# Performance work log

Hardware: AMD Instinct MI355X
Metric: run time of the kernel (lower is better)

## Reference

```python
import jax, jax.numpy as jnp
import numpy as np

C = 256
NUM_HEADS = 4
GROUPS = 32  # max(1, 256//8), divides 256
EPS = 1e-5


def setup_inputs() -> dict:
    key = jax.random.key(0)
    ks = jax.random.split(key, 7)
    B, H, W = 4, 64, 64
    s = 0.02
    return {
        "x": jax.random.normal(ks[0], (B, C, H, W), dtype=jnp.float32),
        "norm_gamma": jnp.ones((C,), jnp.float32),
        "norm_beta": jnp.zeros((C,), jnp.float32),
        "qkv_w": jax.random.normal(ks[1], (3 * C, C), jnp.float32) * s,  # 1x1 conv kernel squeezed
        "qkv_b": jax.random.normal(ks[2], (3 * C,), jnp.float32) * s,
        "proj_w": jax.random.normal(ks[3], (C, C), jnp.float32) * s,
        "proj_b": jax.random.normal(ks[4], (C,), jnp.float32) * s,
    }


def reference(x, norm_gamma, norm_beta, qkv_w, qkv_b, proj_w, proj_b):
    B, Cc, H, W = x.shape
    hd = Cc // NUM_HEADS
    scale = hd ** -0.5

    # GroupNorm over (channels-per-group, H, W)
    xg = x.reshape(B, GROUPS, Cc // GROUPS, H, W)
    mu = xg.mean(axis=(2, 3, 4), keepdims=True)
    var = xg.var(axis=(2, 3, 4), keepdims=True)
    h = ((xg - mu) * jax.lax.rsqrt(var + EPS)).reshape(B, Cc, H, W)
    h = h * norm_gamma[:, None, None] + norm_beta[:, None, None]

    # 1x1 conv QKV: [B,3C,H,W]
    qkv = jnp.einsum('bchw,oc->bohw', h, qkv_w) + qkv_b[:, None, None]
    q, k, v = jnp.split(qkv, 3, axis=1)

    def heads(t):  # [B,C,H,W] -> [B,nh,HW,hd]
        return t.reshape(B, NUM_HEADS, hd, H * W).transpose(0, 1, 3, 2)

    q, k, v = heads(q), heads(k), heads(v)
    attn = jnp.einsum('bhnd,bhmd->bhnm', q, k) * scale  # [B,nh,HW,HW]
    attn = jax.nn.softmax(attn, axis=-1)
    out = jnp.einsum('bhnm,bhmd->bhnd', attn, v)  # [B,nh,HW,hd]
    out = out.transpose(0, 1, 3, 2).reshape(B, Cc, H, W)

    out = jnp.einsum('bchw,oc->bohw', out, proj_w) + proj_b[:, None, None]
    return x + out
```

## Files before the change

kernel.cpp:

```cpp
#include <hip/hip_runtime.h>
#include <hip/hip_bf16.h>
#include <stdint.h>

typedef unsigned short u16;
typedef __attribute__((ext_vector_type(8))) short bf16x8;
typedef __attribute__((ext_vector_type(4))) float f32x4;
typedef __attribute__((ext_vector_type(16))) float f32x16;

#define HW 4096
#define CC 256
#define QSCALE 0.18033688011112042f

__device__ __forceinline__ u16 f2bf(float f) {
    union { float f; uint32_t i; } v; v.f = f;
    uint32_t x = v.i;
    return (u16)((x + 0x7fffu + ((x >> 16) & 1u)) >> 16);
}

__device__ __forceinline__ float fast_exp2(float x) {
#if __has_builtin(__builtin_amdgcn_exp2f)
    return __builtin_amdgcn_exp2f(x);
#else
    return exp2f(x);
#endif
}

__device__ __forceinline__ unsigned cvt_pk_bf16(float lo, float hi) {
    unsigned r;
    asm("v_cvt_pk_bf16_f32 %0, %1, %2" : "=v"(r) : "v"(lo), "v"(hi));
    return r;
}

__device__ __forceinline__ void plane_swap(unsigned& a, unsigned& b) {
#if __has_builtin(__builtin_amdgcn_permlane32_swap)
    auto r = __builtin_amdgcn_permlane32_swap(a, b, false, false);
    a = r[0]; b = r[1];
#else
    unsigned ax = __shfl_xor((int)a, 32);
    unsigned bx = __shfl_xor((int)b, 32);
    bool hi = (threadIdx.x & 32) != 0;
    unsigned na = hi ? bx : a;
    unsigned nb = hi ? b : ax;
    a = na; b = nb;
#endif
}

#define MFMA16(a, b, c) __builtin_amdgcn_mfma_f32_16x16x32_bf16(a, b, c, 0, 0, 0)
#define MFMA32(a, b, c) __builtin_amdgcn_mfma_f32_32x32x16_bf16(a, b, c, 0, 0, 0)

__global__ void k_wsc(const float* __restrict__ qkv_w, const float* __restrict__ proj_w,
                      const float* __restrict__ x,
                      u16* __restrict__ wqkv, u16* __restrict__ wproj, float* __restrict__ stats) {
    int bid = blockIdx.x;
    if (bid < 128) {
        int bg = bid;
        const float4* p = reinterpret_cast<const float4*>(x + (size_t)bg * 8 * HW);
        float s = 0.f, ss = 0.f;
        for (int i = 0; i < 32; ++i) {
            float4 v = p[threadIdx.x + i * 256];
            s += v.x + v.y + v.z + v.w;
            ss += v.x * v.x + v.y * v.y + v.z * v.z + v.w * v.w;
        }
        __shared__ float rs[256], rss[256];
        rs[threadIdx.x] = s; rss[threadIdx.x] = ss;
        __syncthreads();
        for (int off = 128; off > 0; off >>= 1) {
            if (threadIdx.x < off) { rs[threadIdx.x] += rs[threadIdx.x + off]; rss[threadIdx.x] += rss[threadIdx.x + off]; }
            __syncthreads();
        }
        if (threadIdx.x == 0) {
            float mu = rs[0] * (1.f / 32768.f);
            float var = rss[0] * (1.f / 32768.f) - mu * mu;
            stats[bg * 2] = mu;
            stats[bg * 2 + 1] = rsqrtf(var + 1e-5f);
        }
    } else {
        int i = (bid - 128) * 256 + threadIdx.x;
        if (i < 768 * 256) {
            int o = i >> 8;
            float sc = (o < 256) ? QSCALE : 1.0f;
            wqkv[i] = f2bf(qkv_w[i] * sc);
        }
        int j = i - 768 * 256;
        if (j >= 0 && j < 256 * 256) wproj[j] = f2bf(proj_w[j]);
    }
}

__global__ __launch_bounds__(256) void k_gnt(const float* __restrict__ x, const float* __restrict__ stats,
                                             const float* __restrict__ gamma, const float* __restrict__ beta,
                                             u16* __restrict__ h_t) {
    int bid = blockIdx.x;
    int b = bid >> 8;
    int cb = (bid >> 6) & 3;
    int nb = bid & 63;
    int t = threadIdx.x;
    int cl = t >> 2;
    int ch = t & 3;
    int c = cb * 64 + cl;
    int g = c >> 3;
    float mu = stats[(b * 32 + g) * 2];
    float rsg = stats[(b * 32 + g) * 2 + 1];
    float ga = gamma[c], be = beta[c];
    __shared__ float T[64][66];
    const float4* p = reinterpret_cast<const float4*>(x + ((size_t)(b * CC + c)) * HW + nb * 64 + ch * 16);
    for (int j = 0; j < 4; ++j) {
        float4 v = p[j];
        int nbase = ch * 16 + j * 4;
        T[nbase + 0][cl] = (v.x - mu) * rsg * ga + be;
        T[nbase + 1][cl] = (v.y - mu) * rsg * ga + be;
        T[nbase + 2][cl] = (v.z - mu) * rsg * ga + be;
        T[nbase + 3][cl] = (v.w - mu) * rsg * ga + be;
    }
    __syncthreads();
    int nl = t >> 2;
    union { u16 u[16]; uint4 q[2]; } pk;
    for (int j = 0; j < 16; ++j) pk.u[j] = f2bf(T[nl][ch * 16 + j]);
    u16* dst = h_t + ((size_t)b * HW + nb * 64 + nl) * CC + cb * 64 + ch * 16;
    *reinterpret_cast<uint4*>(dst) = pk.q[0];
    *reinterpret_cast<uint4*>(dst + 8) = pk.q[1];
}

__global__ __launch_bounds__(256) void k_qkv(const u16* __restrict__ wqkv, const u16* __restrict__ h_t,
                                             const float* __restrict__ qkv_b,
                                             u16* __restrict__ qk_t, u16* __restrict__ v_o) {
    int bid = blockIdx.x;
    int b = bid / 192;
    int rem = bid % 192;
    int om = rem >> 5;
    int nb = rem & 31;
    int o0 = om * 128, n0 = nb * 128;
    int t = threadIdx.x;
    int wid = t >> 6, lane = t & 63;
    int wm = wid >> 1, wn = wid & 1;
    int l15 = lane & 15, lg = lane >> 4;

    __shared__ u16 sA[128 * 40], sB[128 * 40];
    f32x4 acc[4][4];
    for (int i = 0; i < 4; ++i) for (int j = 0; j < 4; ++j) acc[i][j] = (f32x4)0.f;

    const u16* gA = wqkv + (size_t)o0 * 256;
    const u16* gB = h_t + ((size_t)b * HW + n0) * CC;
    int row = t >> 1, half = t & 1;

    for (int kt = 0; kt < 8; ++kt) {
        __syncthreads();
        {
            const uint4* pa = reinterpret_cast<const uint4*>(gA + (size_t)row * 256 + kt * 32 + half * 16);
            uint4 a0 = pa[0], a1 = pa[1];
            const uint4* pb = reinterpret_cast<const uint4*>(gB + (size_t)row * 256 + kt * 32 + half * 16);
            uint4 b0 = pb[0], b1 = pb[1];
            *reinterpret_cast<uint4*>(&sA[row * 40 + half * 16]) = a0;
            *reinterpret_cast<uint4*>(&sA[row * 40 + half * 16 + 8]) = a1;
            *reinterpret_cast<uint4*>(&sB[row * 40 + half * 16]) = b0;
            *reinterpret_cast<uint4*>(&sB[row * 40 + half * 16 + 8]) = b1;
        }
        __syncthreads();
        bf16x8 af[4], bfr[4];
        for (int mt = 0; mt < 4; ++mt)
            af[mt] = *reinterpret_cast<const bf16x8*>(&sA[(wm * 64 + mt * 16 + l15) * 40 + lg * 8]);
        for (int nt = 0; nt < 4; ++nt)
            bfr[nt] = *reinterpret_cast<const bf16x8*>(&sB[(wn * 64 + nt * 16 + l15) * 40 + lg * 8]);
        for (int mt = 0; mt < 4; ++mt)
            for (int nt = 0; nt < 4; ++nt)
                acc[mt][nt] = MFMA16(af[mt], bfr[nt], acc[mt][nt]);
    }

    if (o0 < 512) {
        for (int mt = 0; mt < 4; ++mt) {
            int ob = o0 + wm * 64 + mt * 16 + lg * 4;
            float bias[4];
            for (int r = 0; r < 4; ++r) {
                int o = ob + r;
                bias[r] = qkv_b[o] * (o < 256 ? QSCALE : 1.0f);
            }
            for (int nt = 0; nt < 4; ++nt) {
                int n = n0 + wn * 64 + nt * 16 + l15;
                union { u16 u[4]; uint2 q; } pk;
                for (int r = 0; r < 4; ++r) pk.u[r] = f2bf(acc[mt][nt][r] + bias[r]);
                *reinterpret_cast<uint2*>(qk_t + ((size_t)b * HW + n) * 512 + ob) = pk.q;
            }
        }
    } else {
        for (int mt = 0; mt < 4; ++mt) {
            int ob = o0 + wm * 64 + mt * 16 + lg * 4;
            for (int nt = 0; nt < 4; ++nt) {
                int n = n0 + wn * 64 + nt * 16 + l15;
                for (int r = 0; r < 4; ++r) {
                    int o = ob + r;
                    float bias = qkv_b[o];
                    v_o[((size_t)b * 256 + (o - 512)) * HW + n] = f2bf(acc[mt][nt][r] + bias);
                }
            }
        }
    }
}

__global__ __launch_bounds__(512, 4) void k_attn(const u16* __restrict__ qk_t, const u16* __restrict__ v_o,
                                                 u16* __restrict__ ao_t) {
    int bid = blockIdx.x;
    int swz = (bid & 7) * 64 + (bid >> 3);
    int qb = swz & 31, head = (swz >> 5) & 3, b = swz >> 7;
    int n0 = qb * 128;
    int t = threadIdx.x;
    int kg = t >> 8;
    int wq = (t >> 6) & 3;
    int lane = t & 63, l31 = lane & 31, h = lane >> 5;

    __shared__ u16 lds[2 * 2 * 2 * 64 * 72];

    const u16* qbase = qk_t + ((size_t)b * HW + n0 + wq * 32 + l31) * 512 + head * 64 + h * 8;
    bf16x8 qf[4];
#pragma unroll
    for (int cs = 0; cs < 4; ++cs) qf[cs] = *reinterpret_cast<const bf16x8*>(qbase + cs * 16);

    const u16* gK = qk_t + (size_t)b * HW * 512 + 256 + head * 64;
    const u16* gV = v_o + ((size_t)b * 256 + head * 64) * (size_t)HW;

    int tIn = t & 255;
    int srow = tIn >> 3, sch = tIn & 7;
    const u16* pk0 = gK + (size_t)(kg * 2048 + srow) * 512 + sch * 8;
    const u16* pk1 = pk0 + 32 * 512;
    const u16* pv0 = gV + (size_t)srow * HW + kg * 2048 + sch * 8;
    const u16* pv1 = pv0 + 32 * HW;
    uint4 rk0 = *reinterpret_cast<const uint4*>(pk0);
    uint4 rk1 = *reinterpret_cast<const uint4*>(pk1);
    uint4 rv0 = *reinterpret_cast<const uint4*>(pv0);
    uint4 rv1 = *reinterpret_cast<const uint4*>(pv1);

    f32x16 o0 = (f32x16)0.f, o1 = (f32x16)0.f;
    float l_run = 0.f;
    u16* gb = lds + kg * 18432;

    for (int ti = 0; ti < 32; ++ti) {
        u16* bK = gb + (ti & 1) * 9216;
        u16* bV = bK + 4608;
        *reinterpret_cast<uint4*>(bK + srow * 72 + sch * 8) = rk0;
        *reinterpret_cast<uint4*>(bK + (srow + 32) * 72 + sch * 8) = rk1;
        *reinterpret_cast<uint4*>(bV + srow * 72 + sch * 8) = rv0;
        *reinterpret_cast<uint4*>(bV + (srow + 32) * 72 + sch * 8) = rv1;
        __syncthreads();

        if (ti < 31) {
            pk0 += 64 * 512; pk1 += 64 * 512; pv0 += 64; pv1 += 64;
            rk0 = *reinterpret_cast<const uint4*>(pk0);
            rk1 = *reinterpret_cast<const uint4*>(pk1);
            rv0 = *reinterpret_cast<const uint4*>(pv0);
            rv1 = *reinterpret_cast<const uint4*>(pv1);
        }

        f32x16 s0 = (f32x16)0.f, s1 = (f32x16)0.f;
        __builtin_amdgcn_s_setprio(1);
#pragma unroll
        for (int cs = 0; cs < 4; ++cs) {
            bf16x8 k0 = *reinterpret_cast<const bf16x8*>(bK + l31 * 72 + cs * 16 + h * 8);
            bf16x8 k1 = *reinterpret_cast<const bf16x8*>(bK + (l31 + 32) * 72 + cs * 16 + h * 8);
            s0 = MFMA32(k0, qf[cs], s0);
            s1 = MFMA32(k1, qf[cs], s1);
        }
        __builtin_amdgcn_s_setprio(0);

        float ps = 0.f;
#pragma unroll
        for (int i = 0; i < 16; ++i) { float e = fast_exp2(s0[i]); s0[i] = e; ps += e; }
#pragma unroll
        for (int i = 0; i < 16; ++i) { float e = fast_exp2(s1[i]); s1[i] = e; ps += e; }
        l_run += ps;

        unsigned dws[2][8];
#pragma unroll
        for (int a = 0; a < 4; ++a) {
            dws[0][2 * a]     = cvt_pk_bf16(s0[4 * a],     s0[4 * a + 1]);
            dws[0][2 * a + 1] = cvt_pk_bf16(s0[4 * a + 2], s0[4 * a + 3]);
            dws[1][2 * a]     = cvt_pk_bf16(s1[4 * a],     s1[4 * a + 1]);
            dws[1][2 * a + 1] = cvt_pk_bf16(s1[4 * a + 2], s1[4 * a + 3]);
        }
        bf16x8 pf[4];
#pragma unroll
        for (int ks = 0; ks < 4; ++ks) {
            int kt = ks >> 1, sf = ks & 1;
            unsigned A0 = dws[kt][4 * sf + 0], B0 = dws[kt][4 * sf + 2];
            unsigned A1 = dws[kt][4 * sf + 1], B1 = dws[kt][4 * sf + 3];
            plane_swap(A0, B0);
            plane_swap(A1, B1);
            union { unsigned d[4]; bf16x8 v; } u;
            u.d[0] = A0; u.d[1] = A1; u.d[2] = B0; u.d[3] = B1;
            pf[ks] = u.v;
        }

        __builtin_amdgcn_s_setprio(1);
#pragma unroll
        for (int ks = 0; ks < 4; ++ks) {
            bf16x8 v0 = *reinterpret_cast<const bf16x8*>(bV + l31 * 72 + ks * 16 + h * 8);
            bf16x8 v1 = *reinterpret_cast<const bf16x8*>(bV + (l31 + 32) * 72 + ks * 16 + h * 8);
            o0 = MFMA32(v0, pf[ks], o0);
            o1 = MFMA32(v1, pf[ks], o1);
        }
        __builtin_amdgcn_s_setprio(0);
    }

    l_run += __shfl_xor(l_run, 32);

    float* Of = (float*)lds;
    float* Lf = (float*)lds + 8192;
    u16* E = lds + 18432;

    __syncthreads();
    if (kg == 1) {
#pragma unroll
        for (int i = 0; i < 16; ++i) {
            Of[wq * 2048 + i * 64 + lane] = o0[i];
            Of[wq * 2048 + (16 + i) * 64 + lane] = o1[i];
        }
        Lf[wq * 64 + lane] = l_run;
    }
    __syncthreads();
    if (kg == 0) {
#pragma unroll
        for (int i = 0; i < 16; ++i) {
            o0[i] += Of[wq * 2048 + i * 64 + lane];
            o1[i] += Of[wq * 2048 + (16 + i) * 64 + lane];
        }
        l_run += Lf[wq * 64 + lane];
        float inv = 1.0f / l_run;
        int qrow = wq * 32 + l31;
#pragma unroll
        for (int r = 0; r < 16; ++r) {
            int d = (r & 3) + 8 * (r >> 2) + 4 * h;
            E[qrow * 72 + d]      = f2bf(o0[r] * inv);
            E[qrow * 72 + 32 + d] = f2bf(o1[r] * inv);
        }
    }
    __syncthreads();
#pragma unroll
    for (int i = 0; i < 2; ++i) {
        int item = i * 512 + t;
        int row = item >> 3, cb = item & 7;
        uint4 w = *reinterpret_cast<const uint4*>(E + row * 72 + cb * 8);
        *reinterpret_cast<uint4*>(ao_t + ((size_t)b * HW + n0 + row) * 256 + head * 64 + cb * 8) = w;
    }
}

__global__ __launch_bounds__(256) void k_proj(const u16* __restrict__ wproj, const u16* __restrict__ ao_t,
                                              const float* __restrict__ proj_b, const float* __restrict__ x,
                                              float* __restrict__ out) {
    int bid = blockIdx.x;
    int b = bid >> 6;
    int om = (bid >> 5) & 1;
    int nb = bid & 31;
    int o0 = om * 128, n0 = nb * 128;
    int t = threadIdx.x;
    int wid = t >> 6, lane = t & 63;
    int wm = wid >> 1, wn = wid & 1;
    int l15 = lane & 15, lg = lane >> 4;

    __shared__ u16 sA[128 * 40], sB[128 * 40];
    f32x4 acc[4][4];
    for (int i = 0; i < 4; ++i) for (int j = 0; j < 4; ++j) acc[i][j] = (f32x4)0.f;

    const u16* gA = wproj + (size_t)o0 * 256;
    const u16* gB = ao_t + ((size_t)b * HW + n0) * CC;
    int row = t >> 1, half = t & 1;

    for (int kt = 0; kt < 8; ++kt) {
        __syncthreads();
        {
            const uint4* pa = reinterpret_cast<const uint4*>(gA + (size_t)row * 256 + kt * 32 + half * 16);
            uint4 a0 = pa[0], a1 = pa[1];
            const uint4* pb = reinterpret_cast<const uint4*>(gB + (size_t)row * 256 + kt * 32 + half * 16);
            uint4 b0 = pb[0], b1 = pb[1];
            *reinterpret_cast<uint4*>(&sA[row * 40 + half * 16]) = a0;
            *reinterpret_cast<uint4*>(&sA[row * 40 + half * 16 + 8]) = a1;
            *reinterpret_cast<uint4*>(&sB[row * 40 + half * 16]) = b0;
            *reinterpret_cast<uint4*>(&sB[row * 40 + half * 16 + 8]) = b1;
        }
        __syncthreads();
        bf16x8 af[4], bfr[4];
        for (int mt = 0; mt < 4; ++mt)
            af[mt] = *reinterpret_cast<const bf16x8*>(&sA[(wm * 64 + mt * 16 + l15) * 40 + lg * 8]);
        for (int nt = 0; nt < 4; ++nt)
            bfr[nt] = *reinterpret_cast<const bf16x8*>(&sB[(wn * 64 + nt * 16 + l15) * 40 + lg * 8]);
        for (int mt = 0; mt < 4; ++mt)
            for (int nt = 0; nt < 4; ++nt)
                acc[mt][nt] = MFMA16(af[mt], bfr[nt], acc[mt][nt]);
    }

    for (int mt = 0; mt < 4; ++mt) {
        int ob = o0 + wm * 64 + mt * 16 + lg * 4;
        for (int nt = 0; nt < 4; ++nt) {
            int n = n0 + wn * 64 + nt * 16 + l15;
            for (int r = 0; r < 4; ++r) {
                int o = ob + r;
                size_t idx = ((size_t)(b * CC + o)) * HW + n;
                out[idx] = acc[mt][nt][r] + proj_b[o] + x[idx];
            }
        }
    }
}

extern "C" void kernel_launch(void* const* d_in, const int* in_sizes, int n_in,
                              void* d_out, int out_size, void* d_ws, size_t ws_size,
                              hipStream_t stream) {
    const float* x      = (const float*)d_in[0];
    const float* gamma  = (const float*)d_in[1];
    const float* beta   = (const float*)d_in[2];
    const float* qkv_w  = (const float*)d_in[3];
    const float* qkv_b  = (const float*)d_in[4];
    const float* proj_w = (const float*)d_in[5];
    const float* proj_b = (const float*)d_in[6];
    float* out = (float*)d_out;
    char* ws = (char*)d_ws;

    float* stats = (float*)ws;
    u16* wqkv  = (u16*)(ws + 4096);
    u16* wproj = (u16*)(ws + 4096 + 393216);
    u16* h_t   = (u16*)(ws + 1048576);
    u16* qk_t  = (u16*)(ws + 1048576 + 8388608);
    u16* v_o   = (u16*)(ws + 1048576 + 8388608 + 16777216);
    u16* ao_t  = (u16*)(ws + 1048576 + 8388608 + 16777216 + 8388608);

    k_wsc<<<dim3(1152), dim3(256), 0, stream>>>(qkv_w, proj_w, x, wqkv, wproj, stats);
    k_gnt<<<dim3(1024), dim3(256), 0, stream>>>(x, stats, gamma, beta, h_t);
    k_qkv<<<dim3(768), dim3(256), 0, stream>>>(wqkv, h_t, qkv_b, qk_t, v_o);
    k_attn<<<dim3(512), dim3(512), 0, stream>>>(qk_t, v_o, ao_t);
    k_proj<<<dim3(256), dim3(256), 0, stream>>>(wproj, ao_t, proj_b, x, out);
}
```

Baseline: 128.9 us.

## Split GroupNorm stats into partial slabs, prefetch V fragments, halve proj tiles

The GroupNorm statistics pass now uses 1024 blocks that each reduce one eighth of a group and write raw partial sums. The normalize kernel combines these partials and computes mean and rsqrt itself, which spreads the reduction over more CUs. In the attention loop, V fragments are loaded from LDS before the QK MFMAs so their latency overlaps with compute. The projection GEMM uses 64-column tiles and 512 blocks to fill more CUs, at the cost of less operand reuse per block.

```diff
diff --git a/kernel.cpp b/kernel.cpp
--- a/kernel.cpp
+++ b/kernel.cpp
@@ -52,11 +52,11 @@
                       const float* __restrict__ x,
                       u16* __restrict__ wqkv, u16* __restrict__ wproj, float* __restrict__ stats) {
     int bid = blockIdx.x;
-    if (bid < 128) {
-        int bg = bid;
-        const float4* p = reinterpret_cast<const float4*>(x + (size_t)bg * 8 * HW);
+    if (bid < 1024) {
+        int bg = bid >> 3, slab = bid & 7;
+        const float4* p = reinterpret_cast<const float4*>(x + (size_t)bg * 32768 + slab * 4096);
         float s = 0.f, ss = 0.f;
-        for (int i = 0; i < 32; ++i) {
+        for (int i = 0; i < 4; ++i) {
             float4 v = p[threadIdx.x + i * 256];
             s += v.x + v.y + v.z + v.w;
             ss += v.x * v.x + v.y * v.y + v.z * v.z + v.w * v.w;
@@ -69,13 +69,11 @@
             __syncthreads();
         }
         if (threadIdx.x == 0) {
-            float mu = rs[0] * (1.f / 32768.f);
-            float var = rss[0] * (1.f / 32768.f) - mu * mu;
-            stats[bg * 2] = mu;
-            stats[bg * 2 + 1] = rsqrtf(var + 1e-5f);
+            stats[bid * 2] = rs[0];
+            stats[bid * 2 + 1] = rss[0];
         }
     } else {
-        int i = (bid - 128) * 256 + threadIdx.x;
+        int i = (bid - 1024) * 256 + threadIdx.x;
         if (i < 768 * 256) {
             int o = i >> 8;
             float sc = (o < 256) ? QSCALE : 1.0f;
@@ -98,8 +96,14 @@
     int ch = t & 3;
     int c = cb * 64 + cl;
     int g = c >> 3;
-    float mu = stats[(b * 32 + g) * 2];
-    float rsg = stats[(b * 32 + g) * 2 + 1];
+    float sum = 0.f, ssum = 0.f;
+    for (int s = 0; s < 8; ++s) {
+        sum  += stats[((b * 32 + g) * 8 + s) * 2];
+        ssum += stats[((b * 32 + g) * 8 + s) * 2 + 1];
+    }
+    float mu = sum * (1.f / 32768.f);
+    float var = ssum * (1.f / 32768.f) - mu * mu;
+    float rsg = rsqrtf(var + 1e-5f);
     float ga = gamma[c], be = beta[c];
     __shared__ float T[64][66];
     const float4* p = reinterpret_cast<const float4*>(x + ((size_t)(b * CC + c)) * HW + nb * 64 + ch * 16);
@@ -248,6 +252,13 @@
             rv1 = *reinterpret_cast<const uint4*>(pv1);
         }
 
+        bf16x8 vfA[4], vfB[4];
+#pragma unroll
+        for (int ks = 0; ks < 4; ++ks) {
+            vfA[ks] = *reinterpret_cast<const bf16x8*>(bV + l31 * 72 + ks * 16 + h * 8);
+            vfB[ks] = *reinterpret_cast<const bf16x8*>(bV + (l31 + 32) * 72 + ks * 16 + h * 8);
+        }
+
         f32x16 s0 = (f32x16)0.f, s1 = (f32x16)0.f;
         __builtin_amdgcn_s_setprio(1);
 #pragma unroll
@@ -290,10 +301,8 @@
         __builtin_amdgcn_s_setprio(1);
 #pragma unroll
         for (int ks = 0; ks < 4; ++ks) {
-            bf16x8 v0 = *reinterpret_cast<const bf16x8*>(bV + l31 * 72 + ks * 16 + h * 8);
-            bf16x8 v1 = *reinterpret_cast<const bf16x8*>(bV + (l31 + 32) * 72 + ks * 16 + h * 8);
-            o0 = MFMA32(v0, pf[ks], o0);
-            o1 = MFMA32(v1, pf[ks], o1);
+            o0 = MFMA32(vfA[ks], pf[ks], o0);
+            o1 = MFMA32(vfB[ks], pf[ks], o1);
         }
         __builtin_amdgcn_s_setprio(0);
     }
@@ -344,50 +353,49 @@
                                               const float* __restrict__ proj_b, const float* __restrict__ x,
                                               float* __restrict__ out) {
     int bid = blockIdx.x;
-    int b = bid >> 6;
-    int om = (bid >> 5) & 1;
-    int nb = bid & 31;
-    int o0 = om * 128, n0 = nb * 128;
+    int b = bid >> 7;
+    int om = (bid >> 6) & 1;
+    int nb = bid & 63;
+    int o0 = om * 128, n0 = nb * 64;
     int t = threadIdx.x;
     int wid = t >> 6, lane = t & 63;
     int wm = wid >> 1, wn = wid & 1;
     int l15 = lane & 15, lg = lane >> 4;
 
-    __shared__ u16 sA[128 * 40], sB[128 * 40];
-    f32x4 acc[4][4];
-    for (int i = 0; i < 4; ++i) for (int j = 0; j < 4; ++j) acc[i][j] = (f32x4)0.f;
+    __shared__ u16 sA[128 * 40], sB[64 * 40];
+    f32x4 acc[4][2];
+    for (int i = 0; i < 4; ++i) for (int j = 0; j < 2; ++j) acc[i][j] = (f32x4)0.f;
 
     const u16* gA = wproj + (size_t)o0 * 256;
     const u16* gB = ao_t + ((size_t)b * HW + n0) * CC;
-    int row = t >> 1, half = t & 1;
+    int rowA = t >> 1, halfA = t & 1;
+    int rowB = t >> 2, qB = t & 3;
 
     for (int kt = 0; kt < 8; ++kt) {
         __syncthreads();
         {
-            const uint4* pa = reinterpret_cast<const uint4*>(gA + (size_t)row * 256 + kt * 32 + half * 16);
+            const uint4* pa = reinterpret_cast<const uint4*>(gA + (size_t)rowA * 256 + kt * 32 + halfA * 16);
             uint4 a0 = pa[0], a1 = pa[1];
-            const uint4* pb = reinterpret_cast<const uint4*>(gB + (size_t)row * 256 + kt * 32 + half * 16);
-            uint4 b0 = pb[0], b1 = pb[1];
-            *reinterpret_cast<uint4*>(&sA[row * 40 + half * 16]) = a0;
-            *reinterpret_cast<uint4*>(&sA[row * 40 + half * 16 + 8]) = a1;
-            *reinterpret_cast<uint4*>(&sB[row * 40 + half * 16]) = b0;
-            *reinterpret_cast<uint4*>(&sB[row * 40 + half * 16 + 8]) = b1;
-        }
-        __syncthreads();
-        bf16x8 af[4], bfr[4];
+            uint4 b0 = *reinterpret_cast<const uint4*>(gB + (size_t)rowB * 256 + kt * 32 + qB * 8);
+            *reinterpret_cast<uint4*>(&sA[rowA * 40 + halfA * 16]) = a0;
+            *reinterpret_cast<uint4*>(&sA[rowA * 40 + halfA * 16 + 8]) = a1;
+            *reinterpret_cast<uint4*>(&sB[rowB * 40 + qB * 8]) = b0;
+        }
+        __syncthreads();
+        bf16x8 af[4], bfr[2];
         for (int mt = 0; mt < 4; ++mt)
             af[mt] = *reinterpret_cast<const bf16x8*>(&sA[(wm * 64 + mt * 16 + l15) * 40 + lg * 8]);
-        for (int nt = 0; nt < 4; ++nt)
-            bfr[nt] = *reinterpret_cast<const bf16x8*>(&sB[(wn * 64 + nt * 16 + l15) * 40 + lg * 8]);
+        for (int nt = 0; nt < 2; ++nt)
+            bfr[nt] = *reinterpret_cast<const bf16x8*>(&sB[(wn * 32 + nt * 16 + l15) * 40 + lg * 8]);
         for (int mt = 0; mt < 4; ++mt)
-            for (int nt = 0; nt < 4; ++nt)
+            for (int nt = 0; nt < 2; ++nt)
                 acc[mt][nt] = MFMA16(af[mt], bfr[nt], acc[mt][nt]);
     }
 
     for (int mt = 0; mt < 4; ++mt) {
         int ob = o0 + wm * 64 + mt * 16 + lg * 4;
-        for (int nt = 0; nt < 4; ++nt) {
-            int n = n0 + wn * 64 + nt * 16 + l15;
+        for (int nt = 0; nt < 2; ++nt) {
+            int n = n0 + wn * 32 + nt * 16 + l15;
             for (int r = 0; r < 4; ++r) {
                 int o = ob + r;
                 size_t idx = ((size_t)(b * CC + o)) * HW + n;
@@ -411,16 +419,16 @@
     char* ws = (char*)d_ws;
 
     float* stats = (float*)ws;
-    u16* wqkv  = (u16*)(ws + 4096);
-    u16* wproj = (u16*)(ws + 4096 + 393216);
+    u16* wqkv  = (u16*)(ws + 8192);
+    u16* wproj = (u16*)(ws + 8192 + 393216);
     u16* h_t   = (u16*)(ws + 1048576);
     u16* qk_t  = (u16*)(ws + 1048576 + 8388608);
     u16* v_o   = (u16*)(ws + 1048576 + 8388608 + 16777216);
     u16* ao_t  = (u16*)(ws + 1048576 + 8388608 + 16777216 + 8388608);
 
-    k_wsc<<<dim3(1152), dim3(256), 0, stream>>>(qkv_w, proj_w, x, wqkv, wproj, stats);
+    k_wsc<<<dim3(2048), dim3(256), 0, stream>>>(qkv_w, proj_w, x, wqkv, wproj, stats);
     k_gnt<<<dim3(1024), dim3(256), 0, stream>>>(x, stats, gamma, beta, h_t);
     k_qkv<<<dim3(768), dim3(256), 0, stream>>>(wqkv, h_t, qkv_b, qk_t, v_o);
     k_attn<<<dim3(512), dim3(512), 0, stream>>>(qk_t, v_o, ao_t);
-    k_proj<<<dim3(256), dim3(256), 0, stream>>>(wproj, ao_t, proj_b, x, out);
-}
+    k_proj<<<dim3(512), dim3(256), 0, stream>>>(wproj, ao_t, proj_b, x, out);
+}
```

After: 290.1 us. 2.25x slower.
